# Performance work log

Hardware: AMD Instinct MI355X
Metric: run time of the kernel (lower is better)

## Reference

```python
import jax, jax.numpy as jnp
import numpy as np

B, S, D, DFF, E, TOPK = 2, 2048, 1024, 2048, 8, 2

def setup_inputs() -> dict:
    key = jax.random.key(0)
    ks = jax.random.split(key, 5)
    scale = 0.02
    return {
        "x": jax.random.normal(ks[0], (B, S, D), dtype=jnp.float32),
        "Wg": jax.random.normal(ks[1], (D, E), dtype=jnp.float32) * scale,
        "bg": jnp.zeros((E,), dtype=jnp.float32),
        "Ww": jax.random.normal(ks[2], (E, D, DFF), dtype=jnp.float32) * scale,
        "bw": jnp.zeros((E, DFF), dtype=jnp.float32),
        "Wv": jax.random.normal(ks[3], (E, D, DFF), dtype=jnp.float32) * scale,
        "bv": jnp.zeros((E, DFF), dtype=jnp.float32),
        "Wo": jax.random.normal(ks[4], (E, DFF, D), dtype=jnp.float32) * scale,
        "bo": jnp.zeros((E, D), dtype=jnp.float32),
    }

def reference(x, Wg, bg, Ww, bw, Wv, bv, Wo, bo):
    b, s, d = x.shape
    t = x.reshape(-1, d)                                  # [N, d]
    # --- router ---
    router_logits = t @ Wg + bg                           # [N, E]
    probs = jax.nn.softmax(router_logits, axis=-1)
    rw, sel = jax.lax.top_k(probs, TOPK)                  # [N, K]
    rw = rw / jnp.sum(rw, axis=-1, keepdims=True)
    # combine weights per (token, expert): zero if expert not selected
    onehot = jax.nn.one_hot(sel, E, dtype=t.dtype)        # [N, K, E]
    cw = jnp.einsum('nk,nke->ne', rw, onehot)             # [N, E]
    # --- experts: dense SwiGLU per expert, weighted combine ---
    wx = jnp.einsum('nd,edf->enf', t, Ww) + bw[:, None, :]  # [E, N, dff]
    vx = jnp.einsum('nd,edf->enf', t, Wv) + bv[:, None, :]
    h = jax.nn.silu(wx) * vx                              # [E, N, dff]
    out_e = jnp.einsum('enf,efd->end', h, Wo) + bo[:, None, :]  # [E, N, d]
    final = jnp.einsum('ne,end->nd', cw, out_e)           # [N, d]
    return final.reshape(b, s, d), router_logits
```

## Files before the change

### kernel.cpp

```cpp
#include <hip/hip_runtime.h>
#include <cstdint>

#define N_TOK 4096
#define DMODEL 1024
#define DFFC 2048
#define NEXP 8
#define NR (N_TOK*2)
#define NRP (NR+256)

typedef unsigned short ushort_t;
typedef __attribute__((ext_vector_type(8))) short short8v;
typedef __attribute__((ext_vector_type(4))) float float4v;

__device__ __forceinline__ ushort_t f2bf(float f){
  union { float f; unsigned u; } v; v.f = f;
  unsigned r = v.u + 0x7fffu + ((v.u >> 16) & 1u);
  return (ushort_t)(r >> 16);
}

__device__ __forceinline__ void gl_lds16(const void* g, void* l){
  __builtin_amdgcn_global_load_lds((const __attribute__((address_space(1))) char*)g,
                                   (__attribute__((address_space(3))) char*)l, 16, 0, 0);
}

__device__ __forceinline__ int frag_off(int row, int slotc){
  return row*64 + ((slotc ^ (row & 7)))*8;
}

__device__ __forceinline__ void fma4(float4& a, float s, float4 q){
  a.x += s*q.x; a.y += s*q.y; a.z += s*q.z; a.w += s*q.w;
}

__global__ __launch_bounds__(256) void router_k(const float* __restrict__ x,
                         const float* __restrict__ Wg, const float* __restrict__ bg,
                         float* __restrict__ logits, int* __restrict__ sel,
                         float* __restrict__ wslot, ushort_t* __restrict__ Xbf){
  int wid = threadIdx.x >> 6;
  int l   = threadIdx.x & 63;
  int t = blockIdx.x*4 + wid;
  const float4* xr = (const float4*)(x + (size_t)t * DMODEL);
  ushort_t* xb = Xbf + (size_t)t * DMODEL;
  float4 acc0 = {0,0,0,0}, acc1 = {0,0,0,0};
  #pragma unroll
  for (int it=0; it<4; ++it){
    int i4 = it*64 + l;
    float4 v = xr[i4];
    const float4* wr4 = (const float4*)(Wg + (size_t)i4*32);
    fma4(acc0, v.x, wr4[0]); fma4(acc1, v.x, wr4[1]);
    fma4(acc0, v.y, wr4[2]); fma4(acc1, v.y, wr4[3]);
    fma4(acc0, v.z, wr4[4]); fma4(acc1, v.z, wr4[5]);
    fma4(acc0, v.w, wr4[6]); fma4(acc1, v.w, wr4[7]);
    ushort4 o; o.x=f2bf(v.x); o.y=f2bf(v.y); o.z=f2bf(v.z); o.w=f2bf(v.w);
    *(ushort4*)(xb + 4*i4) = o;
  }
  float lg[NEXP] = {acc0.x, acc0.y, acc0.z, acc0.w, acc1.x, acc1.y, acc1.z, acc1.w};
  #pragma unroll
  for (int e=0;e<NEXP;e++){
    float v = lg[e];
    #pragma unroll
    for (int s=32;s>0;s>>=1) v += __shfl_xor(v,s);
    lg[e] = v;
  }
  if (l==0){
    float m=-1e30f;
    #pragma unroll
    for (int e=0;e<NEXP;e++){ lg[e]+=bg[e]; m = fmaxf(m,lg[e]); }
    float p[NEXP];
    #pragma unroll
    for (int e=0;e<NEXP;e++) p[e]=__expf(lg[e]-m);
    int e0=0;
    #pragma unroll
    for (int e=1;e<NEXP;e++) if (p[e]>p[e0]) e0=e;
    int e1=(e0==0)?1:0;
    #pragma unroll
    for (int e=0;e<NEXP;e++) if (e!=e0 && p[e]>p[e1]) e1=e;
    float ps=p[e0]+p[e1];
    float4* lgo = (float4*)(logits + (size_t)t*NEXP);
    lgo[0] = make_float4(lg[0],lg[1],lg[2],lg[3]);
    lgo[1] = make_float4(lg[4],lg[5],lg[6],lg[7]);
    sel[t] = e0 | (e1<<8);
    wslot[t*2+0]=p[e0]/ps; wslot[t*2+1]=p[e1]/ps;
  }
}

__global__ __launch_bounds__(256) void build_k(const int* __restrict__ sel,
                                               int* __restrict__ elist, int* __restrict__ cnt){
  int e = blockIdx.x;
  int tid = threadIdx.x;
  int w = tid>>6, l = tid&63;
  __shared__ int wtot[4];
  __shared__ int runbase;
  if (tid==0) runbase = 0;
  __syncthreads();
  unsigned long long lt = (1ULL << l) - 1ULL;
  for (int c=0;c<N_TOK/256;c++){
    int t = c*256 + tid;
    int s = sel[t];
    bool f0 = (s & 255) == e;
    bool f1 = ((s>>8) & 255) == e;
    unsigned long long m0 = __ballot(f0);
    unsigned long long m1 = __ballot(f1);
    int myless = __popcll(m0 & lt) + __popcll(m1 & lt);
    if (l==0) wtot[w] = __popcll(m0) + __popcll(m1);
    __syncthreads();
    int pre = 0, tot = 0;
    #pragma unroll
    for (int j=0;j<4;j++){ if (j<w) pre += wtot[j]; tot += wtot[j]; }
    int base = runbase + pre + myless;
    if (f0) elist[e*N_TOK + base] = 2*t;
    if (f1) elist[e*N_TOK + base + (f0?1:0)] = 2*t + 1;
    __syncthreads();
    if (tid==0) runbase += tot;
    __syncthreads();
  }
  if (tid==0) cnt[e] = runbase;
}

__global__ void scan_k(const int* __restrict__ cnt, int* __restrict__ offs){
  if (threadIdx.x==0 && blockIdx.x==0){
    int s=0;
    for (int e=0;e<NEXP;e++){ offs[e]=s; s+=cnt[e]; }
    offs[NEXP]=s;
  }
}

__global__ void gather_k(const ushort_t* __restrict__ Xbf, const int* __restrict__ offs,
                         const int* __restrict__ elist, const float* __restrict__ wslot,
                         ushort_t* __restrict__ Xg, int* __restrict__ rowslot, float* __restrict__ roww){
  int r = blockIdx.x;
  int e = 0;
  #pragma unroll
  for (int k=1;k<NEXP;k++) if (r >= offs[k]) e = k;
  int i = r - offs[e];
  int entry = elist[e*N_TOK+i];
  int t = entry>>1;
  int tid = threadIdx.x;
  ushort4 v = *(const ushort4*)(Xbf + (size_t)t*DMODEL + tid*4);
  *(ushort4*)(Xg + (size_t)r*DMODEL + tid*4) = v;
  if (tid==0){ rowslot[r]=entry; roww[r]=wslot[entry]; }
}

__global__ void transpose_k(const float* __restrict__ Ww, const float* __restrict__ Wv,
                            const float* __restrict__ Wo,
                            ushort_t* __restrict__ Bcat, ushort_t* __restrict__ WoT){
  __shared__ ushort_t tile[64][68];
  int id = blockIdx.x;
  int e   = id & 7;
  int rem = id >> 3;
  int m   = rem % 3;
  int rest= rem / 3;
  int fx  = rest & 31;
  int ky  = rest >> 5;
  const float* src; int K, F;
  if (m == 0)      { src = Ww + (size_t)e*DMODEL*DFFC; K=DMODEL; F=DFFC; }
  else if (m == 1) { src = Wv + (size_t)e*DMODEL*DFFC; K=DMODEL; F=DFFC; }
  else             { src = Wo + (size_t)e*DFFC*DMODEL; K=DFFC; F=DMODEL; }
  int f0 = fx*64, k0 = ky*64;
  if (f0 >= F || k0 >= K) return;
  int tid = threadIdx.x;
  #pragma unroll
  for (int it=0; it<4; ++it){
    int idx = it*256 + tid;
    int r = idx>>4, c4 = idx&15;
    float4 v = *(const float4*)&src[(size_t)(k0+r)*F + f0 + c4*4];
    ushort4 o; o.x=f2bf(v.x); o.y=f2bf(v.y); o.z=f2bf(v.z); o.w=f2bf(v.w);
    *(ushort4*)&tile[r][c4*4] = o;
  }
  __syncthreads();
  #pragma unroll
  for (int it=0; it<4; ++it){
    int idx = it*256 + tid;
    int c = idx>>4;
    int j = idx&15;
    ushort4 o;
    o.x = tile[4*j+0][c]; o.y = tile[4*j+1][c]; o.z = tile[4*j+2][c]; o.w = tile[4*j+3][c];
    if (m < 2){
      int cc = fx*128 + (c>>4)*32 + m*16 + (c&15);
      *(ushort4*)&Bcat[((size_t)e*4096 + cc)*DMODEL + k0 + 4*j] = o;
    } else {
      *(ushort4*)&WoT[(size_t)e*DMODEL*DFFC + (size_t)(f0+c)*DFFC + k0 + 4*j] = o;
    }
  }
}

__device__ __forceinline__ void stage256(const ushort_t* __restrict__ base, int ldk,
                                         ushort_t* buf, int w, int l){
  int sw = ((l&7) ^ (l>>3))*8;
  #pragma unroll
  for (int j=0;j<4;j++){
    int row = j*32 + w*8 + (l>>3);
    gl_lds16(base + (size_t)row*ldk + sw, &buf[(j*256 + w*64)*8]);
  }
}

__global__ __launch_bounds__(256,4) void gemm1_k(const ushort_t* __restrict__ Xg,
    const ushort_t* __restrict__ Bcat,
    const float* __restrict__ bw, const float* __restrict__ bv,
    const int* __restrict__ cnt, const int* __restrict__ offs,
    ushort_t* __restrict__ H){
  __shared__ ushort_t As[128*64];
  __shared__ ushort_t Bs[128*64];
  int id = blockIdx.x;
  int e  = id & 7;
  int j_ = id >> 3;
  int mt = j_ >> 5;
  int ft = j_ & 31;
  int cnte = cnt[e];
  if (mt*128 >= cnte) return;
  int row0 = offs[e] + mt*128;
  const ushort_t* Ag = Xg   + (size_t)row0*DMODEL;
  const ushort_t* Bg = Bcat + ((size_t)e*4096 + ft*128)*DMODEL;
  int tid = threadIdx.x;
  int w = tid>>6, l = tid&63;
  int wr = w>>1, wc = w&1;

  int aOff[4][2], bOff[4][2];
  #pragma unroll
  for (int m=0;m<4;m++)
    #pragma unroll
    for (int ks=0;ks<2;ks++)
      aOff[m][ks] = frag_off(wr*64 + m*16 + (l&15), ks*4 + (l>>4));
  #pragma unroll
  for (int n=0;n<4;n++)
    #pragma unroll
    for (int ks=0;ks<2;ks++)
      bOff[n][ks] = frag_off(wc*64 + n*16 + (l&15), ks*4 + (l>>4));

  float4v acc[4][4];
  #pragma unroll
  for (int m=0;m<4;m++)
    #pragma unroll
    for (int n=0;n<4;n++) acc[m][n]=(float4v){0,0,0,0};

  const int KT = DMODEL/64;
  for (int kt=0; kt<KT; ++kt){
    stage256(Ag + kt*64, DMODEL, As, w, l);
    stage256(Bg + kt*64, DMODEL, Bs, w, l);
    __syncthreads();
    #pragma unroll
    for (int ks=0; ks<2; ++ks){
      short8v a_[4], b_[4];
      #pragma unroll
      for (int m=0;m<4;m++) a_[m] = *(const short8v*)&As[aOff[m][ks]];
      #pragma unroll
      for (int n=0;n<4;n++) b_[n] = *(const short8v*)&Bs[bOff[n][ks]];
      #pragma unroll
      for (int n=0;n<4;n++)
        #pragma unroll
        for (int m=0;m<4;m++)
          acc[m][n] = __builtin_amdgcn_mfma_f32_16x16x32_bf16(a_[m], b_[n], acc[m][n], 0,0,0);
    }
    __syncthreads();
  }

  int rows_valid = cnte - mt*128; if (rows_valid>128) rows_valid=128;
  #pragma unroll
  for (int m=0;m<4;m++){
    #pragma unroll
    for (int r=0;r<4;r++){
      int row_local = wr*64 + m*16 + (l>>4)*4 + r;
      if (row_local < rows_valid){
        size_t hbase = (size_t)(row0 + row_local)*DFFC;
        #pragma unroll
        for (int np=0;np<2;np++){
          int f = ft*64 + wc*32 + np*16 + (l&15);
          float wx = acc[m][2*np+0][r] + bw[e*DFFC + f];
          float vx = acc[m][2*np+1][r] + bv[e*DFFC + f];
          float h = (wx / (1.f + __expf(-wx))) * vx;
          H[hbase + f] = f2bf(h);
        }
      }
    }
  }
}

__global__ __launch_bounds__(256,4) void gemm2_k(const ushort_t* __restrict__ H,
    const ushort_t* __restrict__ WoT, const float* __restrict__ bo,
    const int* __restrict__ cnt, const int* __restrict__ offs,
    const int* __restrict__ rowslot, const float* __restrict__ roww,
    float* __restrict__ out){
  __shared__ ushort_t As[128*64];
  __shared__ ushort_t Bs[128*64];
  int id = blockIdx.x;
  int e  = id & 7;
  int j_ = id >> 3;
  int mt = j_ >> 3;
  int dt = j_ & 7;
  int cnte = cnt[e];
  if (mt*128 >= cnte) return;
  int row0 = offs[e] + mt*128;
  const ushort_t* Ag = H   + (size_t)row0*DFFC;
  const ushort_t* Bg = WoT + (size_t)e*DMODEL*DFFC + (size_t)(dt*128)*DFFC;
  int tid = threadIdx.x;
  int w = tid>>6, l = tid&63;
  int wr = w>>1, wc = w&1;

  int aOff[4][2], bOff[4][2];
  #pragma unroll
  for (int m=0;m<4;m++)
    #pragma unroll
    for (int ks=0;ks<2;ks++)
      aOff[m][ks] = frag_off(wr*64 + m*16 + (l&15), ks*4 + (l>>4));
  #pragma unroll
  for (int n=0;n<4;n++)
    #pragma unroll
    for (int ks=0;ks<2;ks++)
      bOff[n][ks] = frag_off(wc*64 + n*16 + (l&15), ks*4 + (l>>4));

  float4v acc[4][4];
  #pragma unroll
  for (int m=0;m<4;m++)
    #pragma unroll
    for (int n=0;n<4;n++) acc[m][n]=(float4v){0,0,0,0};

  const int KT = DFFC/64;
  for (int kt=0; kt<KT; ++kt){
    stage256(Ag + kt*64, DFFC, As, w, l);
    stage256(Bg + kt*64, DFFC, Bs, w, l);
    __syncthreads();
    #pragma unroll
    for (int ks=0; ks<2; ++ks){
      short8v a_[4], b_[4];
      #pragma unroll
      for (int m=0;m<4;m++) a_[m] = *(const short8v*)&As[aOff[m][ks]];
      #pragma unroll
      for (int n=0;n<4;n++) b_[n] = *(const short8v*)&Bs[bOff[n][ks]];
      #pragma unroll
      for (int n=0;n<4;n++)
        #pragma unroll
        for (int m=0;m<4;m++)
          acc[m][n] = __builtin_amdgcn_mfma_f32_16x16x32_bf16(a_[m], b_[n], acc[m][n], 0,0,0);
    }
    __syncthreads();
  }

  int rows_valid = cnte - mt*128; if (rows_valid>128) rows_valid=128;
  #pragma unroll
  for (int m=0;m<4;m++){
    #pragma unroll
    for (int r=0;r<4;r++){
      int row_local = wr*64 + m*16 + (l>>4)*4 + r;
      if (row_local < rows_valid){
        int gr = row0 + row_local;
        int entry = rowslot[gr];
        int tk = entry>>1;
        float wgt = roww[gr];
        float* obase = out + (size_t)tk*DMODEL;
        #pragma unroll
        for (int n=0;n<4;n++){
          int d = dt*128 + wc*64 + n*16 + (l&15);
          atomicAdd(&obase[d], wgt * (acc[m][n][r] + bo[e*DMODEL + d]));
        }
      }
    }
  }
}

extern "C" void kernel_launch(void* const* d_in, const int* in_sizes, int n_in,
                              void* d_out, int out_size, void* d_ws, size_t ws_size,
                              hipStream_t stream){
  const float* x   = (const float*)d_in[0];
  const float* Wg  = (const float*)d_in[1];
  const float* bg  = (const float*)d_in[2];
  const float* Ww  = (const float*)d_in[3];
  const float* bwp = (const float*)d_in[4];
  const float* Wv  = (const float*)d_in[5];
  const float* bvp = (const float*)d_in[6];
  const float* Wo  = (const float*)d_in[7];
  const float* bop = (const float*)d_in[8];
  float* out = (float*)d_out;
  float* logits = out + (size_t)N_TOK*DMODEL;

  char* cur = (char*)d_ws;
  auto alloc = [&](size_t b)->char*{ char* p=cur; cur += (b+255)&~(size_t)255; return p; };
  int*      cnt     = (int*)     alloc(NEXP*4);
  int*      offs    = (int*)     alloc((NEXP+1)*4);
  int*      sel     = (int*)     alloc((size_t)N_TOK*4);
  float*    wslot   = (float*)   alloc((size_t)NR*4);
  int*      elist   = (int*)     alloc((size_t)NEXP*N_TOK*4);
  int*      rowslot = (int*)     alloc((size_t)NRP*4);
  float*    roww    = (float*)   alloc((size_t)NRP*4);
  ushort_t* Xbf     = (ushort_t*)alloc((size_t)N_TOK*DMODEL*2);
  ushort_t* Xg      = (ushort_t*)alloc((size_t)NRP*DMODEL*2);
  ushort_t* Hb      = (ushort_t*)alloc((size_t)NRP*DFFC*2);
  ushort_t* Bcat    = (ushort_t*)alloc((size_t)NEXP*2*DFFC*DMODEL*2);
  ushort_t* WoT     = (ushort_t*)alloc((size_t)NEXP*DMODEL*DFFC*2);
  (void)ws_size; (void)in_sizes; (void)n_in; (void)out_size;

  hipMemsetAsync(out, 0, (size_t)N_TOK*DMODEL*4, stream);
  router_k<<<N_TOK/4, 256, 0, stream>>>(x, Wg, bg, logits, sel, wslot, Xbf);
  build_k<<<NEXP, 256, 0, stream>>>(sel, elist, cnt);
  scan_k<<<1, 1, 0, stream>>>(cnt, offs);
  gather_k<<<NR, 256, 0, stream>>>(Xbf, offs, elist, wslot, Xg, rowslot, roww);
  transpose_k<<<NEXP*3*1024, 256, 0, stream>>>(Ww, Wv, Wo, Bcat, WoT);
  gemm1_k<<<NEXP*32*32, 256, 0, stream>>>(Xg, Bcat, bwp, bvp, cnt, offs, Hb);
  gemm2_k<<<NEXP*32*8, 256, 0, stream>>>(Hb, WoT, bop, cnt, offs, rowslot, roww, out);
}
```

Baseline: 273.0 us.

## Fuse token gather into gemm1 A-tile loads and reorder gemm1 block mapping

Drops the separate gather kernel that copied routed token rows into a contiguous buffer. gemm1 now looks up each A-row's token index from the expert list and loads rows straight from the bf16 activations into LDS. gemm2 reads entry and weight from elist/wslot instead of precomputed per-row arrays. The gemm1 block index is also reordered so groups of 4 F-tiles share an M-tile, which may change L2 reuse. This removes one launch and an intermediate write/read, at the cost of scattered row loads and extra index loads.

```diff
diff --git a/kernel.cpp b/kernel.cpp
--- a/kernel.cpp
+++ b/kernel.cpp
@@ -6,7 +6,6 @@
 #define DFFC 2048
 #define NEXP 8
 #define NR (N_TOK*2)
-#define NRP (NR+256)
 
 typedef unsigned short ushort_t;
 typedef __attribute__((ext_vector_type(8))) short short8v;
@@ -124,22 +123,6 @@
   }
 }
 
-__global__ void gather_k(const ushort_t* __restrict__ Xbf, const int* __restrict__ offs,
-                         const int* __restrict__ elist, const float* __restrict__ wslot,
-                         ushort_t* __restrict__ Xg, int* __restrict__ rowslot, float* __restrict__ roww){
-  int r = blockIdx.x;
-  int e = 0;
-  #pragma unroll
-  for (int k=1;k<NEXP;k++) if (r >= offs[k]) e = k;
-  int i = r - offs[e];
-  int entry = elist[e*N_TOK+i];
-  int t = entry>>1;
-  int tid = threadIdx.x;
-  ushort4 v = *(const ushort4*)(Xbf + (size_t)t*DMODEL + tid*4);
-  *(ushort4*)(Xg + (size_t)r*DMODEL + tid*4) = v;
-  if (tid==0){ rowslot[r]=entry; roww[r]=wslot[entry]; }
-}
-
 __global__ void transpose_k(const float* __restrict__ Ww, const float* __restrict__ Wv,
                             const float* __restrict__ Wo,
                             ushort_t* __restrict__ Bcat, ushort_t* __restrict__ WoT){
@@ -193,7 +176,8 @@
   }
 }
 
-__global__ __launch_bounds__(256,4) void gemm1_k(const ushort_t* __restrict__ Xg,
+__global__ __launch_bounds__(256,4) void gemm1_k(const ushort_t* __restrict__ Xbf,
+    const int* __restrict__ elist,
     const ushort_t* __restrict__ Bcat,
     const float* __restrict__ bw, const float* __restrict__ bv,
     const int* __restrict__ cnt, const int* __restrict__ offs,
@@ -203,16 +187,25 @@
   int id = blockIdx.x;
   int e  = id & 7;
   int j_ = id >> 3;
-  int mt = j_ >> 5;
-  int ft = j_ & 31;
+  int fs = j_ >> 7;
+  int mt = (j_ >> 2) & 31;
+  int ft = fs*4 + (j_ & 3);
   int cnte = cnt[e];
   if (mt*128 >= cnte) return;
   int row0 = offs[e] + mt*128;
-  const ushort_t* Ag = Xg   + (size_t)row0*DMODEL;
   const ushort_t* Bg = Bcat + ((size_t)e*4096 + ft*128)*DMODEL;
   int tid = threadIdx.x;
   int w = tid>>6, l = tid&63;
   int wr = w>>1, wc = w&1;
+  int sw = ((l&7) ^ (l>>3))*8;
+
+  int aTok[4];
+  #pragma unroll
+  for (int j=0;j<4;j++){
+    int li = mt*128 + j*32 + w*8 + (l>>3);
+    if (li >= cnte) li = cnte-1;
+    aTok[j] = elist[e*N_TOK + li] >> 1;
+  }
 
   int aOff[4][2], bOff[4][2];
   #pragma unroll
@@ -234,7 +227,9 @@
 
   const int KT = DMODEL/64;
   for (int kt=0; kt<KT; ++kt){
-    stage256(Ag + kt*64, DMODEL, As, w, l);
+    #pragma unroll
+    for (int j=0;j<4;j++)
+      gl_lds16(Xbf + (size_t)aTok[j]*DMODEL + kt*64 + sw, &As[j*2048 + w*512]);
     stage256(Bg + kt*64, DMODEL, Bs, w, l);
     __syncthreads();
     #pragma unroll
@@ -277,7 +272,7 @@
 __global__ __launch_bounds__(256,4) void gemm2_k(const ushort_t* __restrict__ H,
     const ushort_t* __restrict__ WoT, const float* __restrict__ bo,
     const int* __restrict__ cnt, const int* __restrict__ offs,
-    const int* __restrict__ rowslot, const float* __restrict__ roww,
+    const int* __restrict__ elist, const float* __restrict__ wslot,
     float* __restrict__ out){
   __shared__ ushort_t As[128*64];
   __shared__ ushort_t Bs[128*64];
@@ -341,10 +336,10 @@
     for (int r=0;r<4;r++){
       int row_local = wr*64 + m*16 + (l>>4)*4 + r;
       if (row_local < rows_valid){
-        int gr = row0 + row_local;
-        int entry = rowslot[gr];
+        int li = mt*128 + row_local;
+        int entry = elist[e*N_TOK + li];
         int tk = entry>>1;
-        float wgt = roww[gr];
+        float wgt = wslot[entry];
         float* obase = out + (size_t)tk*DMODEL;
         #pragma unroll
         for (int n=0;n<4;n++){
@@ -378,11 +373,8 @@
   int*      sel     = (int*)     alloc((size_t)N_TOK*4);
   float*    wslot   = (float*)   alloc((size_t)NR*4);
   int*      elist   = (int*)     alloc((size_t)NEXP*N_TOK*4);
-  int*      rowslot = (int*)     alloc((size_t)NRP*4);
-  float*    roww    = (float*)   alloc((size_t)NRP*4);
   ushort_t* Xbf     = (ushort_t*)alloc((size_t)N_TOK*DMODEL*2);
-  ushort_t* Xg      = (ushort_t*)alloc((size_t)NRP*DMODEL*2);
-  ushort_t* Hb      = (ushort_t*)alloc((size_t)NRP*DFFC*2);
+  ushort_t* Hb      = (ushort_t*)alloc((size_t)NR*DFFC*2 + 256*DFFC*2);
   ushort_t* Bcat    = (ushort_t*)alloc((size_t)NEXP*2*DFFC*DMODEL*2);
   ushort_t* WoT     = (ushort_t*)alloc((size_t)NEXP*DMODEL*DFFC*2);
   (void)ws_size; (void)in_sizes; (void)n_in; (void)out_size;
@@ -391,8 +383,7 @@
   router_k<<<N_TOK/4, 256, 0, stream>>>(x, Wg, bg, logits, sel, wslot, Xbf);
   build_k<<<NEXP, 256, 0, stream>>>(sel, elist, cnt);
   scan_k<<<1, 1, 0, stream>>>(cnt, offs);
-  gather_k<<<NR, 256, 0, stream>>>(Xbf, offs, elist, wslot, Xg, rowslot, roww);
   transpose_k<<<NEXP*3*1024, 256, 0, stream>>>(Ww, Wv, Wo, Bcat, WoT);
-  gemm1_k<<<NEXP*32*32, 256, 0, stream>>>(Xg, Bcat, bwp, bvp, cnt, offs, Hb);
-  gemm2_k<<<NEXP*32*8, 256, 0, stream>>>(Hb, WoT, bop, cnt, offs, rowslot, roww, out);
-}
+  gemm1_k<<<NEXP*32*32, 256, 0, stream>>>(Xbf, elist, Bcat, bwp, bvp, cnt, offs, Hb);
+  gemm2_k<<<NEXP*32*8, 256, 0, stream>>>(Hb, WoT, bop, cnt, offs, elist, wslot, out);
+}
```

New measurement: 265.7 us. 2.7% less time.
